# Kernel tuning notes

Measured on AMD Instinct MI355X. Metric: run time of the kernel, lower is better.

The kernel has to match this reference:

```python
import jax, jax.numpy as jnp
import numpy as np

N_RAYS = 262144  # 512x512 image
N_PTS = 64       # hardcoded in original forward (reshape(-1, 64, 3))
FAR_DELTA = 1e10 # sentinel delta appended for the last sample


def setup_inputs() -> dict:
    key = jax.random.key(0)
    k1, k2, k3 = jax.random.split(key, 3)
    # non-negative densities, as a density field would produce
    density = jax.random.uniform(k1, (N_RAYS, N_PTS, 1), dtype=jnp.float32)
    # sorted depths along each ray in [2, 6] (typical near/far bounds)
    depth_values = jnp.sort(
        2.0 + 4.0 * jax.random.uniform(k2, (N_RAYS, N_PTS), dtype=jnp.float32),
        axis=-1,
    )
    rays_feature = jax.random.uniform(k3, (N_RAYS, N_PTS, 3), dtype=jnp.float32)
    return {"density": density, "depth_values": depth_values, "rays_feature": rays_feature}


def reference(density, depth_values, rays_feature):
    # deltas: consecutive depth differences, with huge sentinel for last sample
    deltas = jnp.concatenate(
        [depth_values[:, 1:] - depth_values[:, :-1],
         jnp.full_like(depth_values[:, :1], FAR_DELTA)],
        axis=-1,
    )  # (N, P)
    sigma_delta = density[..., 0] * deltas          # (N, P)
    trans_step = jnp.exp(-sigma_delta)              # per-segment transmittance e
    # exclusive cumulative product: T_0 = 1, T_i = prod_{j<i} e_j
    transmittance = jnp.concatenate(
        [jnp.ones_like(trans_step[:, :1]),
         jnp.cumprod(trans_step[:, :-1], axis=1)],
        axis=1,
    )  # (N, P)
    weights = transmittance * (1.0 - trans_step)    # (N, P)
    feature = jnp.sum(weights[..., None] * rays_feature, axis=1)  # (N, 3)
    depth = jnp.sum(weights * depth_values, axis=1)               # (N,)
    return feature, depth
```

## Files before the change

kernel.cpp:

```cpp
#include <hip/hip_runtime.h>
#include <hip/hip_bf16.h>

#define N_RAYS 262144
#define N_PTS  64
#define FAR_DELTA 1e10f
#define RAYS_PER_BLOCK 4

__global__ __launch_bounds__(256) void volume_render_kernel(
    const float* __restrict__ density,
    const float* __restrict__ depth_values,
    const float* __restrict__ rays_feature,
    float* __restrict__ out)
{
    const int wave = threadIdx.x >> 6;
    const int lane = threadIdx.x & 63;
    const int ray  = blockIdx.x * RAYS_PER_BLOCK + wave;
    if (ray >= N_RAYS) return;

    const long base = (long)ray * N_PTS;

    const float d_i  = depth_values[base + lane];
    const float sig  = density[base + lane];

    float d_next = __shfl_down(d_i, 1, 64);
    float delta  = (lane == 63) ? FAR_DELTA : (d_next - d_i);
    float sd     = sig * delta;

    float s = sd;
    #pragma unroll
    for (int off = 1; off < 64; off <<= 1) {
        float t = __shfl_up(s, off, 64);
        if (lane >= off) s += t;
    }
    float s_exc = __shfl_up(s, 1, 64);
    if (lane == 0) s_exc = 0.0f;

    const float e = __expf(-sd);
    const float w = __expf(-s_exc) * (1.0f - e);

    const float* fp = rays_feature + (long)ray * (N_PTS * 3) + lane * 3;
    float wfx = w * fp[0];
    float wfy = w * fp[1];
    float wfz = w * fp[2];
    float wd  = w * d_i;

    #pragma unroll
    for (int off = 32; off > 0; off >>= 1) {
        wfx += __shfl_xor(wfx, off, 64);
        wfy += __shfl_xor(wfy, off, 64);
        wfz += __shfl_xor(wfz, off, 64);
        wd  += __shfl_xor(wd,  off, 64);
    }

    if (lane == 0) {
        out[(long)ray * 3 + 0] = wfx;
        out[(long)ray * 3 + 1] = wfy;
        out[(long)ray * 3 + 2] = wfz;
        out[(long)N_RAYS * 3 + ray] = wd;
    }
}

extern "C" void kernel_launch(void* const* d_in, const int* in_sizes, int n_in,
                              void* d_out, int out_size, void* d_ws, size_t ws_size,
                              hipStream_t stream) {
    const float* density      = (const float*)d_in[0];
    const float* depth_values = (const float*)d_in[1];
    const float* rays_feature = (const float*)d_in[2];
    float* out = (float*)d_out;

    const int blocks = N_RAYS / RAYS_PER_BLOCK;
    volume_render_kernel<<<blocks, 256, 0, stream>>>(
        density, depth_values, rays_feature, out);
}
```

Before: 348.7 us.

## Process four rays per wave with float4 loads and product-based scan

Each wave now handles four rays, with 16 lanes per ray and four samples per lane, loaded as float4 vectors for depth, density and features. The transmittance is built as a local product of four exponentials followed by a 4-step multiplicative scan over 16 lanes, replacing the 6-step additive scan and the extra exp. This reduces shuffle and exp work and widens memory transactions for this memory-bound kernel. Output stores are spread across lanes. The risk is higher register use per lane and slightly different rounding from the product form.

```diff
diff --git a/kernel.cpp b/kernel.cpp
--- a/kernel.cpp
+++ b/kernel.cpp
@@ -1,10 +1,9 @@
 #include <hip/hip_runtime.h>
-#include <hip/hip_bf16.h>
 
 #define N_RAYS 262144
 #define N_PTS  64
 #define FAR_DELTA 1e10f
-#define RAYS_PER_BLOCK 4
+#define RAYS_PER_BLOCK 16
 
 __global__ __launch_bounds__(256) void volume_render_kernel(
     const float* __restrict__ density,
@@ -12,50 +11,66 @@
     const float* __restrict__ rays_feature,
     float* __restrict__ out)
 {
+    const int lane = threadIdx.x & 63;
     const int wave = threadIdx.x >> 6;
-    const int lane = threadIdx.x & 63;
-    const int ray  = blockIdx.x * RAYS_PER_BLOCK + wave;
-    if (ray >= N_RAYS) return;
+    const int sub  = lane >> 4;
+    const int l    = lane & 15;
+    const int ray  = blockIdx.x * RAYS_PER_BLOCK + wave * 4 + sub;
 
-    const long base = (long)ray * N_PTS;
+    const float4 d  = ((const float4*)depth_values)[(long)ray * 16 + l];
+    const float4 sg = ((const float4*)density)[(long)ray * 16 + l];
 
-    const float d_i  = depth_values[base + lane];
-    const float sig  = density[base + lane];
+    const float4* fp = (const float4*)rays_feature + (long)ray * 48 + l * 3;
+    const float4 fa = fp[0];
+    const float4 fb = fp[1];
+    const float4 fc = fp[2];
 
-    float d_next = __shfl_down(d_i, 1, 64);
-    float delta  = (lane == 63) ? FAR_DELTA : (d_next - d_i);
-    float sd     = sig * delta;
+    const float dnx = __shfl_down(d.x, 1, 16);
+    const float dl0 = d.y - d.x;
+    const float dl1 = d.z - d.y;
+    const float dl2 = d.w - d.z;
+    const float dl3 = (l == 15) ? FAR_DELTA : (dnx - d.w);
 
-    float s = sd;
+    const float e0 = __expf(-sg.x * dl0);
+    const float e1 = __expf(-sg.y * dl1);
+    const float e2 = __expf(-sg.z * dl2);
+    const float e3 = __expf(-sg.w * dl3);
+
+    const float q1 = e0;
+    const float q2 = q1 * e1;
+    const float q3 = q2 * e2;
+
+    float ptot = q3 * e3;
     #pragma unroll
-    for (int off = 1; off < 64; off <<= 1) {
-        float t = __shfl_up(s, off, 64);
-        if (lane >= off) s += t;
+    for (int off = 1; off < 16; off <<= 1) {
+        float t = __shfl_up(ptot, off, 16);
+        if (l >= off) ptot *= t;
     }
-    float s_exc = __shfl_up(s, 1, 64);
-    if (lane == 0) s_exc = 0.0f;
+    float p_exc = __shfl_up(ptot, 1, 16);
+    if (l == 0) p_exc = 1.0f;
 
-    const float e = __expf(-sd);
-    const float w = __expf(-s_exc) * (1.0f - e);
+    const float w0 = p_exc *      (1.0f - e0);
+    const float w1 = p_exc * q1 * (1.0f - e1);
+    const float w2 = p_exc * q2 * (1.0f - e2);
+    const float w3 = p_exc * q3 * (1.0f - e3);
 
-    const float* fp = rays_feature + (long)ray * (N_PTS * 3) + lane * 3;
-    float wfx = w * fp[0];
-    float wfy = w * fp[1];
-    float wfz = w * fp[2];
-    float wd  = w * d_i;
+    float fx = w0*fa.x + w1*fa.w + w2*fb.z + w3*fc.y;
+    float fy = w0*fa.y + w1*fb.x + w2*fb.w + w3*fc.z;
+    float fz = w0*fa.z + w1*fb.y + w2*fc.x + w3*fc.w;
+    float wd = w0*d.x  + w1*d.y  + w2*d.z  + w3*d.w;
 
     #pragma unroll
-    for (int off = 32; off > 0; off >>= 1) {
-        wfx += __shfl_xor(wfx, off, 64);
-        wfy += __shfl_xor(wfy, off, 64);
-        wfz += __shfl_xor(wfz, off, 64);
-        wd  += __shfl_xor(wd,  off, 64);
+    for (int off = 8; off > 0; off >>= 1) {
+        fx += __shfl_xor(fx, off, 16);
+        fy += __shfl_xor(fy, off, 16);
+        fz += __shfl_xor(fz, off, 16);
+        wd += __shfl_xor(wd, off, 16);
     }
 
-    if (lane == 0) {
-        out[(long)ray * 3 + 0] = wfx;
-        out[(long)ray * 3 + 1] = wfy;
-        out[(long)ray * 3 + 2] = wfz;
+    if (l < 3) {
+        const float v = (l == 0) ? fx : ((l == 1) ? fy : fz);
+        out[(long)ray * 3 + l] = v;
+    } else if (l == 3) {
         out[(long)N_RAYS * 3 + ray] = wd;
     }
 }
```

Result: no change. 351.2 us (+0.7%).
